# Performance work log

Hardware: AMD Instinct MI355X
Metric: run time of the kernel (lower is better)

The kernel has to match this reference:

```python
import jax, jax.numpy as jnp
import numpy as np

N_NODES = 40000
N_EDGES = 640000
MUL = 32                      # multiplicity of 0e and 1o in node irreps
NUM_NEIGHBORS = 16.0
SILU_NORM = 1.6791767923989418  # e3nn normalize2mom factor for silu
SQRT3 = 3.0 ** 0.5


def setup_inputs() -> dict:
    key = jax.random.key(0)
    ks = jax.random.split(key, 12)
    return {
        "node_input": jax.random.normal(ks[0], (N_NODES, 4 * MUL), dtype=jnp.float32),
        "node_attr": jnp.ones((N_NODES, 1), dtype=jnp.float32),
        "edge_src": jax.random.randint(ks[1], (N_EDGES,), 0, N_NODES, dtype=jnp.int32),
        "edge_dst": jax.random.randint(ks[2], (N_EDGES,), 0, N_NODES, dtype=jnp.int32),
        "edge_attr": jax.random.normal(ks[3], (N_EDGES, 4), dtype=jnp.float32),
        "edge_scalars": jax.random.normal(ks[4], (N_EDGES, 8), dtype=jnp.float32),
        "w_lin1_s": jax.random.normal(ks[5], (MUL, MUL), dtype=jnp.float32),
        "w_lin1_v": jax.random.normal(ks[6], (MUL, MUL), dtype=jnp.float32),
        "fc_w1": jax.random.normal(ks[7], (8, 64), dtype=jnp.float32),
        "fc_w2": jax.random.normal(ks[8], (64, 4 * MUL), dtype=jnp.float32),
        "w_lin2_s": jax.random.normal(ks[9], (2 * MUL, MUL), dtype=jnp.float32),
        "w_lin2_v": jax.random.normal(ks[10], (2 * MUL, MUL), dtype=jnp.float32),
    }


def reference(node_input, node_attr, edge_src, edge_dst, edge_attr, edge_scalars,
              w_lin1_s, w_lin1_v, fc_w1, fc_w2, w_lin2_s, w_lin2_v):
    N = node_input.shape[0]
    # split node features per e3nn layout: [32x0e | 32x1o]
    s = node_input[:, :MUL]                            # [N, 32]
    v = node_input[:, MUL:].reshape(N, MUL, 3)         # [N, 32, 3]

    # linear_1: per-irrep e3nn Linear (weights scaled by 1/sqrt(fan_in))
    s = s @ (w_lin1_s / jnp.sqrt(jnp.float32(MUL)))
    v = jnp.einsum('nui,uw->nwi', v, w_lin1_v / jnp.sqrt(jnp.float32(MUL)))

    # fc: edge_scalars -> tensor-product weights (e3nn FullyConnectedNet, silu)
    h = jax.nn.silu(edge_scalars @ (fc_w1 / jnp.sqrt(jnp.float32(fc_w1.shape[0])))) * SILU_NORM
    w = h @ (fc_w2 / jnp.sqrt(jnp.float32(fc_w2.shape[0])))      # [E, 128]
    w0 = w[:, 0 * MUL:1 * MUL]  # path 0e x 0e -> 0e
    w1 = w[:, 1 * MUL:2 * MUL]  # path 0e x 1o -> 1o
    w2 = w[:, 2 * MUL:3 * MUL]  # path 1o x 0e -> 1o
    w3 = w[:, 3 * MUL:4 * MUL]  # path 1o x 1o -> 0e

    # gather source node features per edge
    se = s[edge_src]            # [E, 32]
    ve = v[edge_src]            # [E, 32, 3]
    es = edge_attr[:, :1]       # [E, 1]  edge 0e
    ev = edge_attr[:, 1:4]      # [E, 3]  edge 1o

    # edge-wise 'uvu' Clebsch-Gordan tensor product (e3nn component-normalized;
    # the sqrt(3) path weight cancels the 1/sqrt(3) of w3j for the l=1 paths)
    mid_s0 = w0 * se * es                                       # 0e x 0e -> 0e
    mid_s1 = w3 * jnp.einsum('eui,ei->eu', ve, ev) / SQRT3      # 1o x 1o -> 0e
    mid_v0 = (w1 * se)[:, :, None] * ev[:, None, :]             # 0e x 1o -> 1o
    mid_v1 = (w2 * es)[:, :, None] * ve                         # 1o x 0e -> 1o
    # sorted irreps_mid layout: [0e(path0), 0e(path3) | 1o(path1), 1o(path2)]
    mid_scal = jnp.concatenate([mid_s0, mid_s1], axis=1)        # [E, 64]
    mid_vec = jnp.concatenate([mid_v0, mid_v1], axis=1)         # [E, 64, 3]

    # scatter-reduce to destination nodes, / sqrt(num_neighbors)
    inv = 1.0 / jnp.sqrt(jnp.float32(NUM_NEIGHBORS))
    ns = jax.ops.segment_sum(mid_scal, edge_dst, num_segments=N) * inv   # [N, 64]
    nv = jax.ops.segment_sum(mid_vec, edge_dst, num_segments=N) * inv    # [N, 64, 3]

    # linear_2: 64x0e+64x1o -> 32x0e+32x1o
    fan = jnp.sqrt(jnp.float32(2 * MUL))
    out_s = ns @ (w_lin2_s / fan)                                # [N, 32]
    out_v = jnp.einsum('nui,uw->nwi', nv, w_lin2_v / fan)        # [N, 32, 3]
    return jnp.concatenate([out_s, out_v.reshape(N, -1)], axis=1)
```

## Files before the change

### kernel.cpp

```cpp
#include <hip/hip_runtime.h>
#include <math.h>

#define NNODES 40000
#define NEDGES 640000
#define NPB 8
#define LROW 257
#define CHUNK 32
#define CHUNK4 16
#define MROW 260
#define NB1 8
#define NB3 8

typedef __attribute__((ext_vector_type(8))) short short8_t;
typedef __attribute__((ext_vector_type(4))) short short4_t;
typedef __attribute__((ext_vector_type(4))) float float4_t;

__device__ __forceinline__ float4 ld4(const float* p) { return *(const float4*)p; }

__device__ __forceinline__ unsigned short bf16r(float x) {
  union { float f; unsigned u; } v; v.f = x;
  unsigned u = v.u;
  u += 0x7FFFu + ((u >> 16) & 1u);
  return (unsigned short)(u >> 16);
}

__device__ __forceinline__ void lds_fadd(float* p, float v) {
  __hip_atomic_fetch_add(p, v, __ATOMIC_RELAXED, __HIP_MEMORY_SCOPE_WORKGROUP);
}

#define INV_SQRT3_C 0.57735026918962576f

__device__ __forceinline__ void accum_half(float* lrow, int u,
    float w0, float w1, float w2, float w3,
    float se, float vx, float vy, float vz,
    float esc, float ev0, float ev1, float ev2) {
  lds_fadd(lrow + u, w0 * se * esc);
  float dv = vx * ev0 + vy * ev1 + vz * ev2;
  lds_fadd(lrow + 32 + u, w3 * dv * INV_SQRT3_C);
  float b1v = w1 * se;
  lds_fadd(lrow + 64 + u * 3 + 0, b1v * ev0);
  lds_fadd(lrow + 64 + u * 3 + 1, b1v * ev1);
  lds_fadd(lrow + 64 + u * 3 + 2, b1v * ev2);
  float b2v = w2 * esc;
  lds_fadd(lrow + 160 + u * 3 + 0, b2v * vx);
  lds_fadd(lrow + 160 + u * 3 + 1, b2v * vy);
  lds_fadd(lrow + 160 + u * 3 + 2, b2v * vz);
}

struct RowData { float se0, se1, vx0, vy0, vz0, vx1, vy1, vz1; };

__device__ __forceinline__ RowData load_row(const float* ab, int m) {
  RowData d;
  d.se0 = ab[m];            d.se1 = ab[m + 16];
  d.vx0 = ab[32 + 3 * m];   d.vy0 = ab[33 + 3 * m];   d.vz0 = ab[34 + 3 * m];
  d.vx1 = ab[80 + 3 * m];   d.vy1 = ab[81 + 3 * m];   d.vz1 = ab[82 + 3 * m];
  return d;
}

__global__ void k1_stage1(const float* __restrict__ node_input,
                          const float* __restrict__ w1s,
                          const float* __restrict__ w1v,
                          float* __restrict__ A) {
  const float scale = 0.17677669529663687f;
  int stride = gridDim.x * blockDim.x;
  for (int idx = blockIdx.x * blockDim.x + threadIdx.x; idx < NNODES * 128; idx += stride) {
    int n = idx >> 7;
    int c = idx & 127;
    const float* row = node_input + n * 128;
    float acc = 0.f;
    if (c < 32) {
      #pragma unroll
      for (int u = 0; u < 32; ++u)
        acc = fmaf(row[u], w1s[u * 32 + c], acc);
    } else {
      int cc = c - 32;
      int w = cc / 3;
      int i = cc - w * 3;
      #pragma unroll
      for (int u = 0; u < 32; ++u)
        acc = fmaf(row[32 + u * 3 + i], w1v[u * 32 + w], acc);
    }
    A[idx] = acc * scale;
  }
}

__global__ __launch_bounds__(256) void k1_stage1b(
    const float* __restrict__ node_input,
    const float* __restrict__ w1s,
    const float* __restrict__ w1v,
    float* __restrict__ A2) {
  __shared__ float rows[NB1 * 128];
  __shared__ float ws[32 * 32];
  __shared__ float wvv[32 * 32];
  const float scale = 0.17677669529663687f;
  int tid = threadIdx.x;
  int n0 = blockIdx.x * NB1;

  float4 a = ((const float4*)w1s)[tid];
  a.x *= scale; a.y *= scale; a.z *= scale; a.w *= scale;
  ((float4*)ws)[tid] = a;
  float4 b = ((const float4*)w1v)[tid];
  b.x *= scale; b.y *= scale; b.z *= scale; b.w *= scale;
  ((float4*)wvv)[tid] = b;
  ((float4*)rows)[tid] = ((const float4*)(node_input + (long)n0 * 128))[tid];
  __syncthreads();

  int j = tid & 31, g = tid >> 5;
  const float* lr = rows + g * 128;
  float ac0 = 0.f, ac1 = 0.f, ac2 = 0.f, ac3 = 0.f;
  #pragma unroll
  for (int t = 0; t < 32; ++t) {
    float wsj = ws[t * 32 + j];
    float wvj = wvv[t * 32 + j];
    ac0 = fmaf(lr[t],            wsj, ac0);
    ac1 = fmaf(lr[32 + 3 * t],     wvj, ac1);
    ac2 = fmaf(lr[32 + 3 * t + 1], wvj, ac2);
    ac3 = fmaf(lr[32 + 3 * t + 2], wvj, ac3);
  }
  float4 o; o.x = ac0; o.y = ac1; o.z = ac2; o.w = ac3;
  ((float4*)(A2 + (long)n0 * 128))[tid] = o;
}

__global__ void k_hist(const int* __restrict__ edge_dst, int* __restrict__ counts) {
  int e = blockIdx.x * blockDim.x + threadIdx.x;
  if (e < NEDGES) atomicAdd(&counts[edge_dst[e]], 1);
}

__global__ void k_scanA(const int* __restrict__ counts, int* __restrict__ bsum) {
  __shared__ int ws[4];
  int t = blockIdx.x * 256 + threadIdx.x;
  int v = (t < NNODES) ? counts[t] : 0;
  for (int d = 32; d; d >>= 1) v += __shfl_down(v, d, 64);
  if ((threadIdx.x & 63) == 0) ws[threadIdx.x >> 6] = v;
  __syncthreads();
  if (threadIdx.x == 0) bsum[blockIdx.x] = ws[0] + ws[1] + ws[2] + ws[3];
}

__global__ __launch_bounds__(256) void k_scanB(const int* __restrict__ bsum,
                                               int* __restrict__ boff,
                                               int* __restrict__ offsets) {
  __shared__ int s[256];
  int tid = threadIdx.x;
  int v = (tid < 157) ? bsum[tid] : 0;
  s[tid] = v;
  __syncthreads();
  for (int d = 1; d < 256; d <<= 1) {
    int x = (tid >= d) ? s[tid - d] : 0;
    __syncthreads();
    s[tid] += x;
    __syncthreads();
  }
  if (tid < 157) boff[tid] = s[tid] - v;
  if (tid == 0) offsets[NNODES] = NEDGES;
}

__global__ __launch_bounds__(256) void k_scanC(const int* __restrict__ counts,
                                               const int* __restrict__ boff,
                                               int* __restrict__ offsets,
                                               int* __restrict__ cursor) {
  __shared__ int s[256];
  int tid = threadIdx.x;
  int t = blockIdx.x * 256 + tid;
  int v = (t < NNODES) ? counts[t] : 0;
  s[tid] = v;
  __syncthreads();
  for (int d = 1; d < 256; d <<= 1) {
    int x = (tid >= d) ? s[tid - d] : 0;
    __syncthreads();
    s[tid] += x;
    __syncthreads();
  }
  int off = boff[blockIdx.x] + s[tid] - v;
  if (t < NNODES) { offsets[t] = off; cursor[t] = off; }
}

__global__ void k_scatter(const int* __restrict__ edge_dst,
                          int* __restrict__ cursor, int* __restrict__ slots) {
  int e = blockIdx.x * blockDim.x + threadIdx.x;
  if (e < NEDGES) {
    int d = edge_dst[e];
    int p = atomicAdd(&cursor[d], 1);
    slots[p] = e;
  }
}

__global__ void k_scatter_pack2(const int* __restrict__ edge_src,
                                const int* __restrict__ edge_dst,
                                const float* __restrict__ edge_attr,
                                const float* __restrict__ edge_scalars,
                                int* __restrict__ cursor,
                                int* __restrict__ PSRC,
                                float4_t* __restrict__ PEA,
                                float4_t* __restrict__ PES) {
  int e = blockIdx.x * blockDim.x + threadIdx.x;
  if (e < NEDGES) {
    int d = edge_dst[e];
    int p = atomicAdd(&cursor[d], 1);
    PSRC[p] = edge_src[e];
    PEA[p] = *(const float4_t*)(edge_attr + (long)e * 4);
    PES[2 * p]     = *(const float4_t*)(edge_scalars + (long)e * 8);
    PES[2 * p + 1] = *(const float4_t*)(edge_scalars + (long)e * 8 + 4);
  }
}

__global__ void k_scatter_pack3(const int* __restrict__ edge_src,
                                const int* __restrict__ edge_dst,
                                const float* __restrict__ edge_attr,
                                const float* __restrict__ edge_scalars,
                                int* __restrict__ cursor,
                                float4_t* __restrict__ PE) {
  int e = blockIdx.x * blockDim.x + threadIdx.x;
  if (e < NEDGES) {
    int d = edge_dst[e];
    int p = atomicAdd(&cursor[d], 1);
    float4_t* b = PE + (long)p * 4;
    b[0] = *(const float4_t*)(edge_attr + (long)e * 4);
    b[1] = *(const float4_t*)(edge_scalars + (long)e * 8);
    b[2] = *(const float4_t*)(edge_scalars + (long)e * 8 + 4);
    float4_t s;
    s.x = __int_as_float(edge_src[e]); s.y = 0.f; s.z = 0.f; s.w = 0.f;
    b[3] = s;
  }
}

__global__ __launch_bounds__(256, 4) void k_edge4b(
    const float* __restrict__ A2,
    const float4_t* __restrict__ PE,
    const float* __restrict__ fc_w1,
    const float* __restrict__ fc_w2,
    const int* __restrict__ offsets,
    float* __restrict__ ACC) {
  const float INV_SQRT8 = 0.35355339059327373f;
  const float H_SCALE   = 1.6791767923989418f / 8.0f;

  __shared__ float  mid[CHUNK4 * MROW];
  __shared__ short  h_lds[CHUNK4 * 72];
  __shared__ float4 w1f[144];

  int tid = threadIdx.x;
  int n0 = blockIdx.x * NPB;
  int ebase = offsets[n0];
  int eend  = offsets[n0 + NPB];

  if (tid < 128) {
    int j = tid >> 1, hf = tid & 1;
    float4 wv4;
    wv4.x = fc_w1[(hf * 4 + 0) * 64 + j] * INV_SQRT8;
    wv4.y = fc_w1[(hf * 4 + 1) * 64 + j] * INV_SQRT8;
    wv4.z = fc_w1[(hf * 4 + 2) * 64 + j] * INV_SQRT8;
    wv4.w = fc_w1[(hf * 4 + 3) * 64 + j] * INV_SQRT8;
    w1f[(j >> 3) * 18 + (j & 7) * 2 + hf] = wv4;
  }

  int wv = tid >> 6;
  int l  = tid & 63;
  int m  = l & 15;
  int q  = l >> 4;
  int uh = wv & 1;
  int cl = wv >> 1;
  int tL = cl * 2 + uh;
  int tH = 4 + cl * 2 + uh;
  int u  = uh * 16 + m;

  short8_t bL0, bL1, bH0, bH1;
  #pragma unroll
  for (int j = 0; j < 8; ++j) {
    bL0[j] = (short)bf16r(fc_w2[(q * 8 + j) * 128      + tL * 16 + m]);
    bL1[j] = (short)bf16r(fc_w2[(32 + q * 8 + j) * 128 + tL * 16 + m]);
    bH0[j] = (short)bf16r(fc_w2[(q * 8 + j) * 128      + tH * 16 + m]);
    bH1[j] = (short)bf16r(fc_w2[(32 + q * 8 + j) * 128 + tH * 16 + m]);
  }

  int nA = 2 * wv;
  int offA0 = offsets[n0 + nA];
  int offA1 = offsets[n0 + nA + 1];
  int offB1 = offsets[n0 + nA + 2];
  float4_t racA = {0.f, 0.f, 0.f, 0.f};
  float4_t racB = {0.f, 0.f, 0.f, 0.f};

  float ea0x, ea0y, ea0z, ea0w, ea1x, ea1y, ea1z, ea1w,
        ea2x, ea2y, ea2z, ea2w, ea3x, ea3y, ea3z, ea3w;
  float se0, se1, se2, se3, vx0, vx1, vx2, vx3,
        vy0, vy1, vy2, vy3, vz0, vz1, vz2, vz3;

  auto loadmeta = [&](int kb) {
    int ecs = kb + m;
    int ecc = (ecs < eend) ? ecs : (eend - 1);
    const float4_t* pb = PE + (long)ecc * 4;
    float4_t eam = pb[0];
    float4_t sA  = pb[1];
    float4_t sB  = pb[2];
    int srcm = __float_as_int(pb[3].x);
    int g  = wv * 2 + (q >> 1);
    int ob = (q & 1) * 4;
    short4_t hq;
    #pragma unroll
    for (int j = 0; j < 4; ++j) {
      float4 wA = w1f[g * 18 + (ob + j) * 2 + 0];
      float4 wB = w1f[g * 18 + (ob + j) * 2 + 1];
      float x = sA.x * wA.x + sA.y * wA.y + sA.z * wA.z + sA.w * wA.w
              + sB.x * wB.x + sB.y * wB.y + sB.z * wB.z + sB.w * wB.w;
      float hv = (x * H_SCALE) / (1.f + __expf(-x));
      hq[j] = (short)bf16r(hv);
    }
    *(short4_t*)((char*)h_lds + m * 144 + wv * 32 + q * 8) = hq;
    int sl0 = q * 4, sl1 = sl0 + 1, sl2 = sl0 + 2, sl3 = sl0 + 3;
    int src0 = __shfl(srcm, sl0, 64), src1 = __shfl(srcm, sl1, 64);
    int src2 = __shfl(srcm, sl2, 64), src3 = __shfl(srcm, sl3, 64);
    ea0x = __shfl(eam.x, sl0, 64); ea0y = __shfl(eam.y, sl0, 64);
    ea0z = __shfl(eam.z, sl0, 64); ea0w = __shfl(eam.w, sl0, 64);
    ea1x = __shfl(eam.x, sl1, 64); ea1y = __shfl(eam.y, sl1, 64);
    ea1z = __shfl(eam.z, sl1, 64); ea1w = __shfl(eam.w, sl1, 64);
    ea2x = __shfl(eam.x, sl2, 64); ea2y = __shfl(eam.y, sl2, 64);
    ea2z = __shfl(eam.z, sl2, 64); ea2w = __shfl(eam.w, sl2, 64);
    ea3x = __shfl(eam.x, sl3, 64); ea3y = __shfl(eam.y, sl3, 64);
    ea3z = __shfl(eam.z, sl3, 64); ea3w = __shfl(eam.w, sl3, 64);
    float4 g0 = *(const float4*)(A2 + (long)src0 * 128 + 4 * u);
    float4 g1 = *(const float4*)(A2 + (long)src1 * 128 + 4 * u);
    float4 g2 = *(const float4*)(A2 + (long)src2 * 128 + 4 * u);
    float4 g3 = *(const float4*)(A2 + (long)src3 * 128 + 4 * u);
    se0 = g0.x; vx0 = g0.y; vy0 = g0.z; vz0 = g0.w;
    se1 = g1.x; vx1 = g1.y; vy1 = g1.z; vz1 = g1.w;
    se2 = g2.x; vx2 = g2.y; vy2 = g2.z; vz2 = g2.w;
    se3 = g3.x; vx3 = g3.y; vy3 = g3.z; vz3 = g3.w;
  };

  __syncthreads();

  if (ebase < eend) {
    loadmeta(ebase);
    for (int k0 = ebase; k0 < eend; k0 += CHUNK4) {
      __syncthreads();
      short8_t a0 = *(const short8_t*)((const char*)h_lds + m * 144 + q * 16);
      short8_t a1 = *(const short8_t*)((const char*)h_lds + m * 144 + 64 + q * 16);
      float4_t acL = {0.f, 0.f, 0.f, 0.f};
      float4_t acH = {0.f, 0.f, 0.f, 0.f};
      acL = __builtin_amdgcn_mfma_f32_16x16x32_bf16(a0, bL0, acL, 0, 0, 0);
      acL = __builtin_amdgcn_mfma_f32_16x16x32_bf16(a1, bL1, acL, 0, 0, 0);
      acH = __builtin_amdgcn_mfma_f32_16x16x32_bf16(a0, bH0, acH, 0, 0, 0);
      acH = __builtin_amdgcn_mfma_f32_16x16x32_bf16(a1, bH1, acH, 0, 0, 0);
#define EPI4(R, SE, VX, VY, VZ, EAX, EAY, EAZ, EAW) do {            \
        float* mrow = mid + (q * 4 + (R)) * MROW;                   \
        if (cl == 0) {                                              \
          mrow[u] = acL[R] * (SE) * (EAX);                          \
          float b = acH[R] * (EAX);                                 \
          mrow[160 + 3 * u + 0] = b * (VX);                         \
          mrow[160 + 3 * u + 1] = b * (VY);                         \
          mrow[160 + 3 * u + 2] = b * (VZ);                         \
        } else {                                                    \
          float dv = (VX) * (EAY) + (VY) * (EAZ) + (VZ) * (EAW);    \
          mrow[32 + u] = acH[R] * dv * INV_SQRT3_C;                 \
          float b = acL[R] * (SE);                                  \
          mrow[64 + 3 * u + 0] = b * (EAY);                         \
          mrow[64 + 3 * u + 1] = b * (EAZ);                         \
          mrow[64 + 3 * u + 2] = b * (EAW);                         \
        }                                                           \
      } while (0)
      EPI4(0, se0, vx0, vy0, vz0, ea0x, ea0y, ea0z, ea0w);
      EPI4(1, se1, vx1, vy1, vz1, ea1x, ea1y, ea1z, ea1w);
      EPI4(2, se2, vx2, vy2, vz2, ea2x, ea2y, ea2z, ea2w);
      EPI4(3, se3, vx3, vy3, vz3, ea3x, ea3y, ea3z, ea3w);
#undef EPI4
      __syncthreads();
      {
        int lo = (offA0 > k0) ? offA0 : k0;
        int hi = offA1 < (k0 + CHUNK4) ? offA1 : (k0 + CHUNK4);
        for (int e = lo; e < hi; ++e) {
          float4_t v = *(const float4_t*)(mid + (e - k0) * MROW + 4 * l);
          racA.x += v.x; racA.y += v.y; racA.z += v.z; racA.w += v.w;
        }
        int lo2 = (offA1 > k0) ? offA1 : k0;
        int hi2 = offB1 < (k0 + CHUNK4) ? offB1 : (k0 + CHUNK4);
        for (int e = lo2; e < hi2; ++e) {
          float4_t v = *(const float4_t*)(mid + (e - k0) * MROW + 4 * l);
          racB.x += v.x; racB.y += v.y; racB.z += v.z; racB.w += v.w;
        }
      }
      if (k0 + CHUNK4 < eend) loadmeta(k0 + CHUNK4);
    }
  }

  *(float4_t*)(ACC + (long)(n0 + nA) * 256 + 4 * l)     = racA;
  *(float4_t*)(ACC + (long)(n0 + nA + 1) * 256 + 4 * l) = racB;
}

__global__ __launch_bounds__(256, 3) void k_edge3(
    const float* __restrict__ A,
    const int* __restrict__ PSRC,
    const float4_t* __restrict__ PEA,
    const float4_t* __restrict__ PES,
    const float* __restrict__ fc_w1,
    const float* __restrict__ fc_w2,
    const int* __restrict__ offsets,
    float* __restrict__ ACC) {
  const float INV_SQRT8 = 0.35355339059327373f;
  const float H_SCALE   = 1.6791767923989418f / 8.0f;

  __shared__ float    mid[CHUNK * MROW];
  __shared__ short8_t w2frag[16 * 64];
  __shared__ float4   w1f[144];

  int tid = threadIdx.x;
  int n0 = blockIdx.x * NPB;
  int ebase = offsets[n0];
  int eend  = offsets[n0 + NPB];

  if (tid < 128) {
    int j = tid >> 1, hf = tid & 1;
    float4 wv4;
    wv4.x = fc_w1[(hf * 4 + 0) * 64 + j] * INV_SQRT8;
    wv4.y = fc_w1[(hf * 4 + 1) * 64 + j] * INV_SQRT8;
    wv4.z = fc_w1[(hf * 4 + 2) * 64 + j] * INV_SQRT8;
    wv4.w = fc_w1[(hf * 4 + 3) * 64 + j] * INV_SQRT8;
    w1f[(j >> 3) * 18 + (j & 7) * 2 + hf] = wv4;
  }
  for (int fi = tid; fi < 16 * 64; fi += 256) {
    int f = fi >> 6, ll = fi & 63;
    int ct = f >> 1, kh = f & 1, mm = ll & 15, qq = ll >> 4;
    short8_t v;
    #pragma unroll
    for (int j = 0; j < 8; ++j)
      v[j] = (short)bf16r(fc_w2[(kh * 32 + qq * 8 + j) * 128 + ct * 16 + mm]);
    w2frag[fi] = v;
  }
  __syncthreads();

  int wv = tid >> 6;
  int l  = tid & 63;
  int m  = l & 15;
  int q  = l >> 4;
  int et = wv & 1;
  int ch = wv >> 1;

  int nA = 2 * wv;
  int offA0 = offsets[n0 + nA];
  int offA1 = offsets[n0 + nA + 1];
  int offB1 = offsets[n0 + nA + 2];
  float4_t racA = {0.f, 0.f, 0.f, 0.f};
  float4_t racB = {0.f, 0.f, 0.f, 0.f};

  for (int k0 = ebase; k0 < eend; k0 += CHUNK) {
    {
      int ecs = k0 + et * 16 + m;
      int ecc = (ecs < eend) ? ecs : (eend - 1);
      int srcm = PSRC[ecc];
      float4 eam = *(const float4*)(PEA + ecc);
      float4 sA  = *(const float4*)(PES + 2 * (long)ecc);
      float4 sB  = *(const float4*)(PES + 2 * (long)ecc + 1);
      float es0 = sA.x, es1 = sA.y, es2 = sA.z, es3 = sA.w;
      float es4 = sB.x, es5 = sB.y, es6 = sB.z, es7 = sB.w;

      short8_t a0, a1;
      #pragma unroll
      for (int jj = 0; jj < 8; ++jj) {
        float4 wA = w1f[q * 18 + jj * 2 + 0];
        float4 wB = w1f[q * 18 + jj * 2 + 1];
        float x = es0 * wA.x + es1 * wA.y + es2 * wA.z + es3 * wA.w
                + es4 * wB.x + es5 * wB.y + es6 * wB.z + es7 * wB.w;
        float hv = (x * H_SCALE) / (1.f + __expf(-x));
        a0[jj] = (short)bf16r(hv);
        float4 wC = w1f[(4 + q) * 18 + jj * 2 + 0];
        float4 wD = w1f[(4 + q) * 18 + jj * 2 + 1];
        float x2 = es0 * wC.x + es1 * wC.y + es2 * wC.z + es3 * wC.w
                 + es4 * wD.x + es5 * wD.y + es6 * wD.z + es7 * wD.w;
        float hv2 = (x2 * H_SCALE) / (1.f + __expf(-x2));
        a1[jj] = (short)bf16r(hv2);
      }

      int sl0 = q * 4, sl1 = sl0 + 1, sl2 = sl0 + 2, sl3 = sl0 + 3;
      int src0 = __shfl(srcm, sl0, 64), src1 = __shfl(srcm, sl1, 64);
      int src2 = __shfl(srcm, sl2, 64), src3 = __shfl(srcm, sl3, 64);
      float ea0x = __shfl(eam.x, sl0, 64), ea0y = __shfl(eam.y, sl0, 64),
            ea0z = __shfl(eam.z, sl0, 64), ea0w = __shfl(eam.w, sl0, 64);
      float ea1x = __shfl(eam.x, sl1, 64), ea1y = __shfl(eam.y, sl1, 64),
            ea1z = __shfl(eam.z, sl1, 64), ea1w = __shfl(eam.w, sl1, 64);
      float ea2x = __shfl(eam.x, sl2, 64), ea2y = __shfl(eam.y, sl2, 64),
            ea2z = __shfl(eam.z, sl2, 64), ea2w = __shfl(eam.w, sl2, 64);
      float ea3x = __shfl(eam.x, sl3, 64), ea3y = __shfl(eam.y, sl3, 64),
            ea3z = __shfl(eam.z, sl3, 64), ea3w = __shfl(eam.w, sl3, 64);

      RowData d0 = load_row(A + (long)src0 * 128, m);
      RowData d1 = load_row(A + (long)src1 * 128, m);
      RowData d2 = load_row(A + (long)src2 * 128, m);
      RowData d3 = load_row(A + (long)src3 * 128, m);

      float4_t acL[2], acH[2];
      #pragma unroll
      for (int uo = 0; uo < 2; ++uo) {
        int tl = ch * 2 + uo;
        short8_t bl0 = w2frag[(tl * 2 + 0) * 64 + l];
        short8_t bl1 = w2frag[(tl * 2 + 1) * 64 + l];
        float4_t zl = (float4_t){0.f, 0.f, 0.f, 0.f};
        zl = __builtin_amdgcn_mfma_f32_16x16x32_bf16(a0, bl0, zl, 0, 0, 0);
        zl = __builtin_amdgcn_mfma_f32_16x16x32_bf16(a1, bl1, zl, 0, 0, 0);
        acL[uo] = zl;
        int th = 4 + ch * 2 + uo;
        short8_t bh0 = w2frag[(th * 2 + 0) * 64 + l];
        short8_t bh1 = w2frag[(th * 2 + 1) * 64 + l];
        float4_t zh = (float4_t){0.f, 0.f, 0.f, 0.f};
        zh = __builtin_amdgcn_mfma_f32_16x16x32_bf16(a0, bh0, zh, 0, 0, 0);
        zh = __builtin_amdgcn_mfma_f32_16x16x32_bf16(a1, bh1, zh, 0, 0, 0);
        acH[uo] = zh;
      }

#define EPI(R, D, EAX, EAY, EAZ, EAW) do {                                       \
        float* mrow = mid + (et * 16 + q * 4 + (R)) * MROW;                      \
        { float wAa = acL[0][R], wBb = acH[0][R];                                \
          if (ch == 0) {                                                         \
            mrow[m] = wAa * D.se0 * EAX;                                         \
            float b = wBb * EAX;                                                 \
            mrow[160 + 3 * m + 0] = b * D.vx0;                                   \
            mrow[160 + 3 * m + 1] = b * D.vy0;                                   \
            mrow[160 + 3 * m + 2] = b * D.vz0;                                   \
          } else {                                                               \
            float dv = D.vx0 * EAY + D.vy0 * EAZ + D.vz0 * EAW;                  \
            mrow[32 + m] = wBb * dv * INV_SQRT3_C;                               \
            float b = wAa * D.se0;                                               \
            mrow[64 + 3 * m + 0] = b * EAY;                                      \
            mrow[64 + 3 * m + 1] = b * EAZ;                                      \
            mrow[64 + 3 * m + 2] = b * EAW;                                      \
          } }                                                                    \
        { float wAa = acL[1][R], wBb = acH[1][R];                                \
          int uu = 16 + m;                                                       \
          if (ch == 0) {                                                         \
            mrow[uu] = wAa * D.se1 * EAX;                                        \
            float b = wBb * EAX;                                                 \
            mrow[160 + 3 * uu + 0] = b * D.vx1;                                  \
            mrow[160 + 3 * uu + 1] = b * D.vy1;                                  \
            mrow[160 + 3 * uu + 2] = b * D.vz1;                                  \
          } else {                                                               \
            float dv = D.vx1 * EAY + D.vy1 * EAZ + D.vz1 * EAW;                  \
            mrow[32 + uu] = wBb * dv * INV_SQRT3_C;                              \
            float b = wAa * D.se1;                                               \
            mrow[64 + 3 * uu + 0] = b * EAY;                                     \
            mrow[64 + 3 * uu + 1] = b * EAZ;                                     \
            mrow[64 + 3 * uu + 2] = b * EAW;                                     \
          } }                                                                    \
      } while (0)

      EPI(0, d0, ea0x, ea0y, ea0z, ea0w);
      EPI(1, d1, ea1x, ea1y, ea1z, ea1w);
      EPI(2, d2, ea2x, ea2y, ea2z, ea2w);
      EPI(3, d3, ea3x, ea3y, ea3z, ea3w);
#undef EPI
    }
    __syncthreads();

    {
      int lo = (offA0 > k0) ? offA0 : k0;
      int hiA = offA1 < (k0 + CHUNK) ? offA1 : (k0 + CHUNK);
      for (int e = lo; e < hiA; ++e) {
        float4_t v = *(const float4_t*)(mid + (e - k0) * MROW + 4 * l);
        racA.x += v.x; racA.y += v.y; racA.z += v.z; racA.w += v.w;
      }
      int lo2 = (offA1 > k0) ? offA1 : k0;
      int hiB = offB1 < (k0 + CHUNK) ? offB1 : (k0 + CHUNK);
      for (int e = lo2; e < hiB; ++e) {
        float4_t v = *(const float4_t*)(mid + (e - k0) * MROW + 4 * l);
        racB.x += v.x; racB.y += v.y; racB.z += v.z; racB.w += v.w;
      }
    }
    __syncthreads();
  }

  *(float4_t*)(ACC + (long)(n0 + nA) * 256 + 4 * l)     = racA;
  *(float4_t*)(ACC + (long)(n0 + nA + 1) * 256 + 4 * l) = racB;
}

__global__ __launch_bounds__(256, 4) void k_edge_fb(
    const float* __restrict__ A,
    const int* __restrict__ edge_src,
    const int* __restrict__ edge_dst,
    const float* __restrict__ edge_attr,
    const float* __restrict__ edge_scalars,
    const float* __restrict__ fc_w1,
    const float* __restrict__ fc_w2,
    const int* __restrict__ offsets,
    const int* __restrict__ slots,
    float* __restrict__ ACC) {
  const float INV_SQRT8 = 0.35355339059327373f;
  const float H_SCALE   = 1.6791767923989418f / 8.0f;

  __shared__ float    lacc[NPB * LROW];
  __shared__ short8_t w2frag[16 * 64];
  __shared__ float4   w1f[144];

  int tid = threadIdx.x;
  int n0 = blockIdx.x * NPB;
  int ebase = offsets[n0];
  int eend  = offsets[n0 + NPB];

  for (int i = tid; i < NPB * LROW; i += 256) lacc[i] = 0.f;
  if (tid < 128) {
    int j = tid >> 1, hf = tid & 1;
    float4 wv4;
    wv4.x = fc_w1[(hf * 4 + 0) * 64 + j] * INV_SQRT8;
    wv4.y = fc_w1[(hf * 4 + 1) * 64 + j] * INV_SQRT8;
    wv4.z = fc_w1[(hf * 4 + 2) * 64 + j] * INV_SQRT8;
    wv4.w = fc_w1[(hf * 4 + 3) * 64 + j] * INV_SQRT8;
    w1f[(j >> 3) * 18 + (j & 7) * 2 + hf] = wv4;
  }
  for (int fi = tid; fi < 16 * 64; fi += 256) {
    int f = fi >> 6, ll = fi & 63;
    int ct = f >> 1, kh = f & 1, mm = ll & 15, qq = ll >> 4;
    short8_t v;
    #pragma unroll
    for (int j = 0; j < 8; ++j)
      v[j] = (short)bf16r(fc_w2[(kh * 32 + qq * 8 + j) * 128 + ct * 16 + mm]);
    w2frag[fi] = v;
  }
  __syncthreads();

  int wv = tid >> 6;
  int l  = tid & 63;
  int m  = l & 15;
  int q  = l >> 4;

  for (int k0 = ebase; k0 < eend; k0 += 64) {
    int ce = k0 + 4 * m + wv;
    bool vld = ce < eend;
    int e = slots[vld ? ce : (eend - 1)];
    int srcm = edge_src[e];
    int lnm  = edge_dst[e] - n0;
    float4 eam = ld4(edge_attr + (long)e * 4);
    float4 sA = ld4(edge_scalars + (long)e * 8);
    float4 sB = ld4(edge_scalars + (long)e * 8 + 4);
    float es0 = sA.x, es1 = sA.y, es2 = sA.z, es3 = sA.w;
    float es4 = sB.x, es5 = sB.y, es6 = sB.z, es7 = sB.w;

    short8_t a0, a1;
    #pragma unroll
    for (int jj = 0; jj < 8; ++jj) {
      float4 wA = w1f[q * 18 + jj * 2 + 0];
      float4 wB = w1f[q * 18 + jj * 2 + 1];
      float x = es0 * wA.x + es1 * wA.y + es2 * wA.z + es3 * wA.w
              + es4 * wB.x + es5 * wB.y + es6 * wB.z + es7 * wB.w;
      float hv = vld ? (x * H_SCALE) / (1.f + __expf(-x)) : 0.f;
      a0[jj] = (short)bf16r(hv);
      float4 wC = w1f[(4 + q) * 18 + jj * 2 + 0];
      float4 wD = w1f[(4 + q) * 18 + jj * 2 + 1];
      float x2 = es0 * wC.x + es1 * wC.y + es2 * wC.z + es3 * wC.w
               + es4 * wD.x + es5 * wD.y + es6 * wD.z + es7 * wD.w;
      float hv2 = vld ? (x2 * H_SCALE) / (1.f + __expf(-x2)) : 0.f;
      a1[jj] = (short)bf16r(hv2);
    }

    int sl0 = q * 4, sl1 = sl0 + 1, sl2 = sl0 + 2, sl3 = sl0 + 3;
    int src0 = __shfl(srcm, sl0, 64), src1 = __shfl(srcm, sl1, 64);
    int src2 = __shfl(srcm, sl2, 64), src3 = __shfl(srcm, sl3, 64);
    int ln0 = __shfl(lnm, sl0, 64), ln1 = __shfl(lnm, sl1, 64);
    int ln2 = __shfl(lnm, sl2, 64), ln3 = __shfl(lnm, sl3, 64);
    float ea0x = __shfl(eam.x, sl0, 64), ea0y = __shfl(eam.y, sl0, 64),
          ea0z = __shfl(eam.z, sl0, 64), ea0w = __shfl(eam.w, sl0, 64);
    float ea1x = __shfl(eam.x, sl1, 64), ea1y = __shfl(eam.y, sl1, 64),
          ea1z = __shfl(eam.z, sl1, 64), ea1w = __shfl(eam.w, sl1, 64);
    float ea2x = __shfl(eam.x, sl2, 64), ea2y = __shfl(eam.y, sl2, 64),
          ea2z = __shfl(eam.z, sl2, 64), ea2w = __shfl(eam.w, sl2, 64);
    float ea3x = __shfl(eam.x, sl3, 64), ea3y = __shfl(eam.y, sl3, 64),
          ea3z = __shfl(eam.z, sl3, 64), ea3w = __shfl(eam.w, sl3, 64);

    const float* abA = A + (long)src0 * 128;
    const float* abB = A + (long)src1 * 128;
    RowData dA = load_row(abA, m);
    RowData dB = load_row(abB, m);

    float4_t acc[8];
    #pragma unroll
    for (int t = 0; t < 8; ++t) {
      short8_t b0 = w2frag[(t * 2 + 0) * 64 + l];
      short8_t b1 = w2frag[(t * 2 + 1) * 64 + l];
      float4_t z = (float4_t){0.f, 0.f, 0.f, 0.f};
      z = __builtin_amdgcn_mfma_f32_16x16x32_bf16(a0, b0, z, 0, 0, 0);
      z = __builtin_amdgcn_mfma_f32_16x16x32_bf16(a1, b1, z, 0, 0, 0);
      acc[t] = z;
    }

    const float* abC = A + (long)src2 * 128;
    const float* abD = A + (long)src3 * 128;
    RowData dC = load_row(abC, m);
    RowData dD = load_row(abD, m);

    #define ACCUM_ROW(RR, LN, EAX, EAY, EAZ, EAW, D) do {                        \
        float* lrow = lacc + (LN) * LROW;                                        \
        accum_half(lrow, m,      acc[0][RR], acc[2][RR], acc[4][RR], acc[6][RR], \
                   D.se0, D.vx0, D.vy0, D.vz0, EAX, EAY, EAZ, EAW);              \
        accum_half(lrow, m + 16, acc[1][RR], acc[3][RR], acc[5][RR], acc[7][RR], \
                   D.se1, D.vx1, D.vy1, D.vz1, EAX, EAY, EAZ, EAW);              \
      } while (0)

    if (k0 + 64 <= eend) {
      ACCUM_ROW(0, ln0, ea0x, ea0y, ea0z, ea0w, dA);
      ACCUM_ROW(1, ln1, ea1x, ea1y, ea1z, ea1w, dB);
      ACCUM_ROW(2, ln2, ea2x, ea2y, ea2z, ea2w, dC);
      ACCUM_ROW(3, ln3, ea3x, ea3y, ea3z, ea3w, dD);
    } else {
      int cb = k0 + 16 * q + wv;
      if (cb + 0  < eend) ACCUM_ROW(0, ln0, ea0x, ea0y, ea0z, ea0w, dA);
      if (cb + 4  < eend) ACCUM_ROW(1, ln1, ea1x, ea1y, ea1z, ea1w, dB);
      if (cb + 8  < eend) ACCUM_ROW(2, ln2, ea2x, ea2y, ea2z, ea2w, dC);
      if (cb + 12 < eend) ACCUM_ROW(3, ln3, ea3x, ea3y, ea3z, ea3w, dD);
    }
    #undef ACCUM_ROW
  }
  __syncthreads();

  for (int i = tid; i < NPB * 256; i += 256) {
    int node = i >> 8;
    int c = i & 255;
    ACC[(long)(n0 + node) * 256 + c] = lacc[node * LROW + c];
  }
}

__global__ void k3_stage2(const float* __restrict__ ACC,
                          const float* __restrict__ w2s,
                          const float* __restrict__ w2v,
                          float* __restrict__ out) {
  const float scale = 0.03125f;
  int stride = gridDim.x * blockDim.x;
  for (int idx = blockIdx.x * blockDim.x + threadIdx.x; idx < NNODES * 128; idx += stride) {
    int n = idx >> 7;
    int c = idx & 127;
    const float* row = ACC + (long)n * 256;
    float acc = 0.f;
    if (c < 32) {
      #pragma unroll
      for (int qq = 0; qq < 64; ++qq)
        acc = fmaf(row[qq], w2s[qq * 32 + c], acc);
    } else {
      int cc = c - 32;
      int w = cc / 3;
      int i = cc - w * 3;
      #pragma unroll
      for (int qq = 0; qq < 64; ++qq)
        acc = fmaf(row[64 + qq * 3 + i], w2v[qq * 32 + w], acc);
    }
    out[idx] = acc * scale;
  }
}

__global__ __launch_bounds__(256) void k3_stage2b(
    const float* __restrict__ ACC,
    const float* __restrict__ w2s,
    const float* __restrict__ w2v,
    float* __restrict__ out) {
  __shared__ float rows[NB3 * 256];
  __shared__ float ws[64 * 32];
  __shared__ float wvv[64 * 32];
  const float scale = 0.03125f;
  int tid = threadIdx.x;
  int n0 = blockIdx.x * NB3;

  #pragma unroll
  for (int k = 0; k < 2; ++k) {
    int i = tid + k * 256;
    float4 a = ((const float4*)w2s)[i];
    a.x *= scale; a.y *= scale; a.z *= scale; a.w *= scale;
    ((float4*)ws)[i] = a;
    float4 b = ((const float4*)w2v)[i];
    b.x *= scale; b.y *= scale; b.z *= scale; b.w *= scale;
    ((float4*)wvv)[i] = b;
    ((float4*)rows)[i] = ((const float4*)(ACC + (long)n0 * 256))[i];
  }
  __syncthreads();

  int j = tid & 31, g = tid >> 5;
  const float* lr = rows + g * 256;
  float ac0 = 0.f, ac1 = 0.f, ac2 = 0.f, ac3 = 0.f;
  #pragma unroll
  for (int t = 0; t < 64; ++t) {
    float wsj = ws[t * 32 + j];
    float wvj = wvv[t * 32 + j];
    ac0 = fmaf(lr[t],            wsj, ac0);
    ac1 = fmaf(lr[64 + 3 * t],     wvj, ac1);
    ac2 = fmaf(lr[64 + 3 * t + 1], wvj, ac2);
    ac3 = fmaf(lr[64 + 3 * t + 2], wvj, ac3);
  }
  float* po = out + (long)(n0 + g) * 128;
  po[j] = ac0;
  po[32 + 3 * j + 0] = ac1;
  po[32 + 3 * j + 1] = ac2;
  po[32 + 3 * j + 2] = ac3;
}

extern "C" void kernel_launch(void* const* d_in, const int* in_sizes, int n_in,
                              void* d_out, int out_size, void* d_ws, size_t ws_size,
                              hipStream_t stream) {
  const float* node_input   = (const float*)d_in[0];
  const int*   edge_src     = (const int*)d_in[2];
  const int*   edge_dst     = (const int*)d_in[3];
  const float* edge_attr    = (const float*)d_in[4];
  const float* edge_scalars = (const float*)d_in[5];
  const float* fc_w1        = (const float*)d_in[8];
  const float* fc_w2        = (const float*)d_in[9];
  const float* w_lin1_s     = (const float*)d_in[6];
  const float* w_lin1_v     = (const float*)d_in[7];
  const float* w_lin2_s     = (const float*)d_in[10];
  const float* w_lin2_v     = (const float*)d_in[11];

  float* out = (float*)d_out;
  float* Abuf = out;

  const size_t SZ_ACC = (size_t)NNODES * 256 * sizeof(float);
  const size_t SZ_PE  = (size_t)NEDGES * 64;
  const size_t SZ_PES = (size_t)NEDGES * 32;
  const size_t SZ_PEA = (size_t)NEDGES * 16;
  const size_t SZ_PSR = (size_t)NEDGES * 4;
  const size_t SZ_CNT = (size_t)NNODES * sizeof(int);
  const size_t SZ_OFF = (size_t)(NNODES + 4) * sizeof(int);
  const size_t SZ_SLT = (size_t)NEDGES * sizeof(int);
  const size_t need1 = SZ_ACC + SZ_PE + 3 * SZ_CNT + SZ_OFF + 2048;
  const size_t need2 = SZ_ACC + SZ_PES + SZ_PEA + SZ_PSR + 3 * SZ_CNT + SZ_OFF + 2048;

  if (ws_size >= need1) {
    char* p = (char*)d_ws;
    float*    ACC = (float*)p;    p += SZ_ACC;
    float4_t* PE  = (float4_t*)p; p += SZ_PE;
    int* counts   = (int*)p;      p += SZ_CNT;
    int* offsets  = (int*)p;      p += SZ_OFF;
    int* cursor   = (int*)p;      p += SZ_CNT;
    int* bsum     = (int*)p;      p += 160 * sizeof(int);
    int* boff     = (int*)p;      p += 160 * sizeof(int);

    hipMemsetAsync(counts, 0, SZ_CNT, stream);
    k1_stage1b<<<NNODES / NB1, 256, 0, stream>>>(node_input, w_lin1_s, w_lin1_v, Abuf);
    k_hist<<<NEDGES / 256, 256, 0, stream>>>(edge_dst, counts);
    k_scanA<<<157, 256, 0, stream>>>(counts, bsum);
    k_scanB<<<1, 256, 0, stream>>>(bsum, boff, offsets);
    k_scanC<<<157, 256, 0, stream>>>(counts, boff, offsets, cursor);
    k_scatter_pack3<<<NEDGES / 256, 256, 0, stream>>>(edge_src, edge_dst, edge_attr,
                                                      edge_scalars, cursor, PE);
    k_edge4b<<<NNODES / NPB, 256, 0, stream>>>(Abuf, PE, fc_w1, fc_w2, offsets, ACC);
    k3_stage2b<<<NNODES / NB3, 256, 0, stream>>>(ACC, w_lin2_s, w_lin2_v, out);
  } else if (ws_size >= need2) {
    char* p = (char*)d_ws;
    float*    ACC = (float*)p;    p += SZ_ACC;
    float4_t* PES = (float4_t*)p; p += SZ_PES;
    float4_t* PEA = (float4_t*)p; p += SZ_PEA;
    int*      PSRC = (int*)p;     p += SZ_PSR;
    int* counts   = (int*)p;      p += SZ_CNT;
    int* offsets  = (int*)p;      p += SZ_OFF;
    int* cursor   = (int*)p;      p += SZ_CNT;
    int* bsum     = (int*)p;      p += 160 * sizeof(int);
    int* boff     = (int*)p;      p += 160 * sizeof(int);

    hipMemsetAsync(counts, 0, SZ_CNT, stream);
    k1_stage1<<<2048, 256, 0, stream>>>(node_input, w_lin1_s, w_lin1_v, Abuf);
    k_hist<<<NEDGES / 256, 256, 0, stream>>>(edge_dst, counts);
    k_scanA<<<157, 256, 0, stream>>>(counts, bsum);
    k_scanB<<<1, 256, 0, stream>>>(bsum, boff, offsets);
    k_scanC<<<157, 256, 0, stream>>>(counts, boff, offsets, cursor);
    k_scatter_pack2<<<NEDGES / 256, 256, 0, stream>>>(edge_src, edge_dst, edge_attr,
                                                      edge_scalars, cursor, PSRC, PEA, PES);
    k_edge3<<<NNODES / NPB, 256, 0, stream>>>(Abuf, PSRC, PEA, PES, fc_w1, fc_w2,
                                              offsets, ACC);
    k3_stage2<<<2048, 256, 0, stream>>>(ACC, w_lin2_s, w_lin2_v, out);
  } else {
    char* p = (char*)d_ws;
    float* ACC    = (float*)p;  p += SZ_ACC;
    int* counts   = (int*)p;    p += SZ_CNT;
    int* offsets  = (int*)p;    p += SZ_OFF;
    int* cursor   = (int*)p;    p += SZ_CNT;
    int* slots    = (int*)p;    p += SZ_SLT;
    int* bsum     = (int*)p;    p += 160 * sizeof(int);
    int* boff     = (int*)p;    p += 160 * sizeof(int);

    hipMemsetAsync(counts, 0, SZ_CNT, stream);
    k1_stage1<<<2048, 256, 0, stream>>>(node_input, w_lin1_s, w_lin1_v, Abuf);
    k_hist<<<NEDGES / 256, 256, 0, stream>>>(edge_dst, counts);
    k_scanA<<<157, 256, 0, stream>>>(counts, bsum);
    k_scanB<<<1, 256, 0, stream>>>(bsum, boff, offsets);
    k_scanC<<<157, 256, 0, stream>>>(counts, boff, offsets, cursor);
    k_scatter<<<NEDGES / 256, 256, 0, stream>>>(edge_dst, cursor, slots);
    k_edge_fb<<<NNODES / NPB, 256, 0, stream>>>(Abuf, edge_src, edge_dst, edge_attr,
                                                edge_scalars, fc_w1, fc_w2,
                                                offsets, slots, ACC);
    k3_stage2<<<2048, 256, 0, stream>>>(ACC, w_lin2_s, w_lin2_v, out);
  }
}
```

Baseline: 337.1 us.

## Fuse linear_2 into edge kernel, merge scan stages, load edge metadata directly

```diff
diff --git a/kernel.cpp b/kernel.cpp
--- a/kernel.cpp
+++ b/kernel.cpp
@@ -174,6 +174,39 @@
   if (t < NNODES) { offsets[t] = off; cursor[t] = off; }
 }
 
+__global__ __launch_bounds__(256) void k_scanBC(
+    const int* __restrict__ counts,
+    const int* __restrict__ bsum,
+    int* __restrict__ offsets,
+    int* __restrict__ cursor) {
+  __shared__ int sb[256];
+  __shared__ int s[256];
+  int tid = threadIdx.x;
+  int vb = (tid < 157) ? bsum[tid] : 0;
+  sb[tid] = vb;
+  __syncthreads();
+  for (int d = 1; d < 256; d <<= 1) {
+    int x = (tid >= d) ? sb[tid - d] : 0;
+    __syncthreads();
+    sb[tid] += x;
+    __syncthreads();
+  }
+  int myboff = (blockIdx.x == 0) ? 0 : sb[blockIdx.x - 1];
+  int t = blockIdx.x * 256 + tid;
+  int v = (t < NNODES) ? counts[t] : 0;
+  s[tid] = v;
+  __syncthreads();
+  for (int d = 1; d < 256; d <<= 1) {
+    int x = (tid >= d) ? s[tid - d] : 0;
+    __syncthreads();
+    s[tid] += x;
+    __syncthreads();
+  }
+  int off = myboff + s[tid] - v;
+  if (t < NNODES) { offsets[t] = off; cursor[t] = off; }
+  if (blockIdx.x == 0 && tid == 0) offsets[NNODES] = NEDGES;
+}
+
 __global__ void k_scatter(const int* __restrict__ edge_dst,
                           int* __restrict__ cursor, int* __restrict__ slots) {
   int e = blockIdx.x * blockDim.x + threadIdx.x;
@@ -223,19 +256,24 @@
   }
 }
 
-__global__ __launch_bounds__(256, 4) void k_edge4b(
+__global__ __launch_bounds__(256, 4) void k_edge5(
     const float* __restrict__ A2,
     const float4_t* __restrict__ PE,
     const float* __restrict__ fc_w1,
     const float* __restrict__ fc_w2,
+    const float* __restrict__ w2s,
+    const float* __restrict__ w2v,
     const int* __restrict__ offsets,
-    float* __restrict__ ACC) {
+    float* __restrict__ out) {
   const float INV_SQRT8 = 0.35355339059327373f;
   const float H_SCALE   = 1.6791767923989418f / 8.0f;
+  const float S2SCALE   = 0.03125f;
 
   __shared__ float  mid[CHUNK4 * MROW];
   __shared__ short  h_lds[CHUNK4 * 72];
   __shared__ float4 w1f[144];
+  __shared__ float  ws2[64 * 32];
+  __shared__ float  wv2[64 * 32];
 
   int tid = threadIdx.x;
   int n0 = blockIdx.x * NPB;
@@ -250,6 +288,16 @@
     wv4.z = fc_w1[(hf * 4 + 2) * 64 + j] * INV_SQRT8;
     wv4.w = fc_w1[(hf * 4 + 3) * 64 + j] * INV_SQRT8;
     w1f[(j >> 3) * 18 + (j & 7) * 2 + hf] = wv4;
+  }
+  #pragma unroll
+  for (int k = 0; k < 2; ++k) {
+    int i = tid + k * 256;
+    float4 a = ((const float4*)w2s)[i];
+    a.x *= S2SCALE; a.y *= S2SCALE; a.z *= S2SCALE; a.w *= S2SCALE;
+    ((float4*)ws2)[i] = a;
+    float4 b = ((const float4*)w2v)[i];
+    b.x *= S2SCALE; b.y *= S2SCALE; b.z *= S2SCALE; b.w *= S2SCALE;
+    ((float4*)wv2)[i] = b;
   }
 
   int wv = tid >> 6;
@@ -287,10 +335,8 @@
     int ecs = kb + m;
     int ecc = (ecs < eend) ? ecs : (eend - 1);
     const float4_t* pb = PE + (long)ecc * 4;
-    float4_t eam = pb[0];
     float4_t sA  = pb[1];
     float4_t sB  = pb[2];
-    int srcm = __float_as_int(pb[3].x);
     int g  = wv * 2 + (q >> 1);
     int ob = (q & 1) * 4;
     short4_t hq;
@@ -304,21 +350,27 @@
       hq[j] = (short)bf16r(hv);
     }
     *(short4_t*)((char*)h_lds + m * 144 + wv * 32 + q * 8) = hq;
-    int sl0 = q * 4, sl1 = sl0 + 1, sl2 = sl0 + 2, sl3 = sl0 + 3;
-    int src0 = __shfl(srcm, sl0, 64), src1 = __shfl(srcm, sl1, 64);
-    int src2 = __shfl(srcm, sl2, 64), src3 = __shfl(srcm, sl3, 64);
-    ea0x = __shfl(eam.x, sl0, 64); ea0y = __shfl(eam.y, sl0, 64);
-    ea0z = __shfl(eam.z, sl0, 64); ea0w = __shfl(eam.w, sl0, 64);
-    ea1x = __shfl(eam.x, sl1, 64); ea1y = __shfl(eam.y, sl1, 64);
-    ea1z = __shfl(eam.z, sl1, 64); ea1w = __shfl(eam.w, sl1, 64);
-    ea2x = __shfl(eam.x, sl2, 64); ea2y = __shfl(eam.y, sl2, 64);
-    ea2z = __shfl(eam.z, sl2, 64); ea2w = __shfl(eam.w, sl2, 64);
-    ea3x = __shfl(eam.x, sl3, 64); ea3y = __shfl(eam.y, sl3, 64);
-    ea3z = __shfl(eam.z, sl3, 64); ea3w = __shfl(eam.w, sl3, 64);
-    float4 g0 = *(const float4*)(A2 + (long)src0 * 128 + 4 * u);
-    float4 g1 = *(const float4*)(A2 + (long)src1 * 128 + 4 * u);
-    float4 g2 = *(const float4*)(A2 + (long)src2 * 128 + 4 * u);
-    float4 g3 = *(const float4*)(A2 + (long)src3 * 128 + 4 * u);
+    int eb = kb + q * 4;
+    int e0 = (eb     < eend) ? eb     : (eend - 1);
+    int e1 = (eb + 1 < eend) ? eb + 1 : (eend - 1);
+    int e2 = (eb + 2 < eend) ? eb + 2 : (eend - 1);
+    int e3 = (eb + 3 < eend) ? eb + 3 : (eend - 1);
+    const float4_t* p0 = PE + (long)e0 * 4;
+    const float4_t* p1 = PE + (long)e1 * 4;
+    const float4_t* p2 = PE + (long)e2 * 4;
+    const float4_t* p3 = PE + (long)e3 * 4;
+    float4_t a0v = p0[0]; int s0i = __float_as_int(p0[3].x);
+    float4_t a1v = p1[0]; int s1i = __float_as_int(p1[3].x);
+    float4_t a2v = p2[0]; int s2i = __float_as_int(p2[3].x);
+    float4_t a3v = p3[0]; int s3i = __float_as_int(p3[3].x);
+    ea0x = a0v.x; ea0y = a0v.y; ea0z = a0v.z; ea0w = a0v.w;
+    ea1x = a1v.x; ea1y = a1v.y; ea1z = a1v.z; ea1w = a1v.w;
+    ea2x = a2v.x; ea2y = a2v.y; ea2z = a2v.z; ea2w = a2v.w;
+    ea3x = a3v.x; ea3y = a3v.y; ea3z = a3v.z; ea3w = a3v.w;
+    float4 g0 = *(const float4*)(A2 + (long)s0i * 128 + 4 * u);
+    float4 g1 = *(const float4*)(A2 + (long)s1i * 128 + 4 * u);
+    float4 g2 = *(const float4*)(A2 + (long)s2i * 128 + 4 * u);
+    float4 g3 = *(const float4*)(A2 + (long)s3i * 128 + 4 * u);
     se0 = g0.x; vx0 = g0.y; vy0 = g0.z; vz0 = g0.w;
     se1 = g1.x; vx1 = g1.y; vy1 = g1.z; vz1 = g1.w;
     se2 = g2.x; vx2 = g2.y; vy2 = g2.z; vz2 = g2.w;
@@ -380,8 +432,29 @@
     }
   }
 
-  *(float4_t*)(ACC + (long)(n0 + nA) * 256 + 4 * l)     = racA;
-  *(float4_t*)(ACC + (long)(n0 + nA + 1) * 256 + 4 * l) = racB;
+  __syncthreads();
+  *(float4_t*)(mid + (2 * wv) * MROW + 4 * l)     = racA;
+  *(float4_t*)(mid + (2 * wv + 1) * MROW + 4 * l) = racB;
+  __syncthreads();
+  {
+    int j = tid & 31, g = tid >> 5;
+    const float* nr = mid + g * MROW;
+    float ac0 = 0.f, ac1 = 0.f, ac2 = 0.f, ac3 = 0.f;
+    #pragma unroll
+    for (int t = 0; t < 64; ++t) {
+      float wsj = ws2[t * 32 + j];
+      float wvj = wv2[t * 32 + j];
+      ac0 = fmaf(nr[t],              wsj, ac0);
+      ac1 = fmaf(nr[64 + 3 * t],     wvj, ac1);
+      ac2 = fmaf(nr[64 + 3 * t + 1], wvj, ac2);
+      ac3 = fmaf(nr[64 + 3 * t + 2], wvj, ac3);
+    }
+    float* po = out + (long)(n0 + g) * 128;
+    po[j] = ac0;
+    po[32 + 3 * j + 0] = ac1;
+    po[32 + 3 * j + 1] = ac2;
+    po[32 + 3 * j + 2] = ac3;
+  }
 }
 
 __global__ __launch_bounds__(256, 3) void k_edge3(
@@ -738,50 +811,6 @@
   }
 }
 
-__global__ __launch_bounds__(256) void k3_stage2b(
-    const float* __restrict__ ACC,
-    const float* __restrict__ w2s,
-    const float* __restrict__ w2v,
-    float* __restrict__ out) {
-  __shared__ float rows[NB3 * 256];
-  __shared__ float ws[64 * 32];
-  __shared__ float wvv[64 * 32];
-  const float scale = 0.03125f;
-  int tid = threadIdx.x;
-  int n0 = blockIdx.x * NB3;
-
-  #pragma unroll
-  for (int k = 0; k < 2; ++k) {
-    int i = tid + k * 256;
-    float4 a = ((const float4*)w2s)[i];
-    a.x *= scale; a.y *= scale; a.z *= scale; a.w *= scale;
-    ((float4*)ws)[i] = a;
-    float4 b = ((const float4*)w2v)[i];
-    b.x *= scale; b.y *= scale; b.z *= scale; b.w *= scale;
-    ((float4*)wvv)[i] = b;
-    ((float4*)rows)[i] = ((const float4*)(ACC + (long)n0 * 256))[i];
-  }
-  __syncthreads();
-
-  int j = tid & 31, g = tid >> 5;
-  const float* lr = rows + g * 256;
-  float ac0 = 0.f, ac1 = 0.f, ac2 = 0.f, ac3 = 0.f;
-  #pragma unroll
-  for (int t = 0; t < 64; ++t) {
-    float wsj = ws[t * 32 + j];
-    float wvj = wvv[t * 32 + j];
-    ac0 = fmaf(lr[t],            wsj, ac0);
-    ac1 = fmaf(lr[64 + 3 * t],     wvj, ac1);
-    ac2 = fmaf(lr[64 + 3 * t + 1], wvj, ac2);
-    ac3 = fmaf(lr[64 + 3 * t + 2], wvj, ac3);
-  }
-  float* po = out + (long)(n0 + g) * 128;
-  po[j] = ac0;
-  po[32 + 3 * j + 0] = ac1;
-  po[32 + 3 * j + 1] = ac2;
-  po[32 + 3 * j + 2] = ac3;
-}
-
 extern "C" void kernel_launch(void* const* d_in, const int* in_sizes, int n_in,
                               void* d_out, int out_size, void* d_ws, size_t ws_size,
                               hipStream_t stream) {
@@ -798,9 +827,9 @@
   const float* w_lin2_v     = (const float*)d_in[11];
 
   float* out = (float*)d_out;
-  float* Abuf = out;
 
   const size_t SZ_ACC = (size_t)NNODES * 256 * sizeof(float);
+  const size_t SZ_A2  = (size_t)NNODES * 128 * sizeof(float);
   const size_t SZ_PE  = (size_t)NEDGES * 64;
   const size_t SZ_PES = (size_t)NEDGES * 32;
   const size_t SZ_PEA = (size_t)NEDGES * 16;
@@ -808,30 +837,31 @@
   const size_t SZ_CNT = (size_t)NNODES * sizeof(int);
   const size_t SZ_OFF = (size_t)(NNODES + 4) * sizeof(int);
   const size_t SZ_SLT = (size_t)NEDGES * sizeof(int);
-  const size_t need1 = SZ_ACC + SZ_PE + 3 * SZ_CNT + SZ_OFF + 2048;
+  const size_t need1 = SZ_A2 + SZ_PE + 3 * SZ_CNT + SZ_OFF + 2048;
   const size_t need2 = SZ_ACC + SZ_PES + SZ_PEA + SZ_PSR + 3 * SZ_CNT + SZ_OFF + 2048;
 
   if (ws_size >= need1) {
     char* p = (char*)d_ws;
-    float*    ACC = (float*)p;    p += SZ_ACC;
+    float*    A2  = (float*)p;    p += SZ_A2;
     float4_t* PE  = (float4_t*)p; p += SZ_PE;
     int* counts   = (int*)p;      p += SZ_CNT;
     int* offsets  = (int*)p;      p += SZ_OFF;
     int* cursor   = (int*)p;      p += SZ_CNT;
     int* bsum     = (int*)p;      p += 160 * sizeof(int);
     int* boff     = (int*)p;      p += 160 * sizeof(int);
+    (void)boff;
 
     hipMemsetAsync(counts, 0, SZ_CNT, stream);
-    k1_stage1b<<<NNODES / NB1, 256, 0, stream>>>(node_input, w_lin1_s, w_lin1_v, Abuf);
+    k1_stage1b<<<NNODES / NB1, 256, 0, stream>>>(node_input, w_lin1_s, w_lin1_v, A2);
     k_hist<<<NEDGES / 256, 256, 0, stream>>>(edge_dst, counts);
     k_scanA<<<157, 256, 0, stream>>>(counts, bsum);
-    k_scanB<<<1, 256, 0, stream>>>(bsum, boff, offsets);
-    k_scanC<<<157, 256, 0, stream>>>(counts, boff, offsets, cursor);
+    k_scanBC<<<157, 256, 0, stream>>>(counts, bsum, offsets, cursor);
     k_scatter_pack3<<<NEDGES / 256, 256, 0, stream>>>(edge_src, edge_dst, edge_attr,
                                                       edge_scalars, cursor, PE);
-    k_edge4b<<<NNODES / NPB, 256, 0, stream>>>(Abuf, PE, fc_w1, fc_w2, offsets, ACC);
-    k3_stage2b<<<NNODES / NB3, 256, 0, stream>>>(ACC, w_lin2_s, w_lin2_v, out);
+    k_edge5<<<NNODES / NPB, 256, 0, stream>>>(A2, PE, fc_w1, fc_w2,
+                                              w_lin2_s, w_lin2_v, offsets, out);
   } else if (ws_size >= need2) {
+    float* Abuf = out;
     char* p = (char*)d_ws;
     float*    ACC = (float*)p;    p += SZ_ACC;
     float4_t* PES = (float4_t*)p; p += SZ_PES;
@@ -855,6 +885,7 @@
                                               offsets, ACC);
     k3_stage2<<<2048, 256, 0, stream>>>(ACC, w_lin2_s, w_lin2_v, out);
   } else {
+    float* Abuf = out;
     char* p = (char*)d_ws;
     float* ACC    = (float*)p;  p += SZ_ACC;
     int* counts   = (int*)p;    p += SZ_CNT;
```

Result: faster. 322.7 us (-4.3%).
